# Kernel tuning notes

Hardware: AMD Instinct MI355X
Metric: run time of the kernel (lower is better)

## Reference

```python
import jax, jax.numpy as jnp
import numpy as np

B = 16; DEMO = 5; COND = 50; QOI = 50
L = DEMO * (COND + 2 * QOI)  # 750
D = 1024; H = 16; HD = D // H; NL = 6; DFF = 4096
IN_DIM = 5; OUT_DIM = 2; MAXPOS = max(COND, QOI)
NEG = -1e9


def _build_consts():
    # token types per demo segment: 0=cond, 1=qoi_kv, 2=qoi_k (query)
    types, demo, pos = [], [], []
    for d in range(DEMO):
        types += [0] * COND + [1] * QOI + [2] * QOI
        demo += [d] * (COND + 2 * QOI)
        pos += list(range(COND)) + list(range(QOI)) + list(range(QOI))
    t = np.array(types); g = np.array(demo); p = np.array(pos)
    ti, tj = t[:, None], t[None, :]
    gi, gj = g[:, None], g[None, :]
    eye = np.arange(L)[:, None] == np.arange(L)[None, :]
    prev = (gj < gi) & (tj < 2)                      # attend to cond/qoi_kv of earlier demos
    same = (gj == gi) & ((tj == 0) | ((ti == 1) & (tj == 1)) | ((ti == 2) & eye))
    mask = prev | same                               # True = allowed
    out_idx = np.where(t == 2)[0]                    # qoi_k positions -> outputs
    return mask, p, out_idx


def setup_inputs():
    key = jax.random.key(0)
    ks = jax.random.split(key, 10)
    mask, pos, out_idx = _build_consts()
    s = 0.02
    return {
        'sequence': jax.random.normal(ks[0], (B, L, IN_DIM), jnp.float32),
        'pre_W': jax.random.normal(ks[1], (IN_DIM, D), jnp.float32) * s,
        'pre_b': jnp.zeros((D,), jnp.float32),
        'pe_table': jax.random.normal(ks[2], (MAXPOS, D), jnp.float32) * s,
        'Wqkv': jax.random.normal(ks[3], (NL, D, 3 * D), jnp.float32) * s,
        'bqkv': jnp.zeros((NL, 3 * D), jnp.float32),
        'Wo': jax.random.normal(ks[4], (NL, D, D), jnp.float32) * s,
        'bo': jnp.zeros((NL, D), jnp.float32),
        'ln1_g': jnp.ones((NL, D), jnp.float32), 'ln1_b': jnp.zeros((NL, D), jnp.float32),
        'ln2_g': jnp.ones((NL, D), jnp.float32), 'ln2_b': jnp.zeros((NL, D), jnp.float32),
        'W1': jax.random.normal(ks[5], (NL, D, DFF), jnp.float32) * s,
        'b1': jnp.zeros((NL, DFF), jnp.float32),
        'W2': jax.random.normal(ks[6], (NL, DFF, D), jnp.float32) * s,
        'b2': jnp.zeros((NL, D), jnp.float32),
        'post_W': jax.random.normal(ks[7], (D, OUT_DIM), jnp.float32) * s,
        'post_b': jnp.zeros((OUT_DIM,), jnp.float32),
        'basic_mask': jnp.asarray(mask),
        'index_pos': jnp.asarray(pos, jnp.int32),
        'out_idx': jnp.asarray(out_idx, jnp.int32),
    }


def _ln(x, g, b):
    m = jnp.mean(x, axis=-1, keepdims=True)
    v = jnp.var(x, axis=-1, keepdims=True)
    return (x - m) * jax.lax.rsqrt(v + 1e-5) * g + b


def _encoder(x, bias, Wqkv, bqkv, Wo, bo, ln1_g, ln1_b, ln2_g, ln2_b, W1, b1, W2, b2):
    scale = 1.0 / np.sqrt(HD)
    for l in range(NL):
        qkv = x @ Wqkv[l] + bqkv[l]                          # [B,L,3D]
        q, k, v = jnp.split(qkv, 3, axis=-1)
        hd = lambda t: t.reshape(B, L, H, HD).transpose(0, 2, 1, 3)
        q, k, v = hd(q), hd(k), hd(v)
        sc = jnp.einsum('bhqd,bhkd->bhqk', q, k) * scale + bias
        a = jax.nn.softmax(sc, axis=-1)
        o = jnp.einsum('bhqk,bhkd->bhqd', a, v).transpose(0, 2, 1, 3).reshape(B, L, D)
        x = _ln(x + o @ Wo[l] + bo[l], ln1_g[l], ln1_b[l])   # post-LN (torch default)
        h = jax.nn.gelu(x @ W1[l] + b1[l], approximate=False)
        x = _ln(x + h @ W2[l] + b2[l], ln2_g[l], ln2_b[l])
    return x


def reference(sequence, pre_W, pre_b, pe_table, Wqkv, bqkv, Wo, bo,
              ln1_g, ln1_b, ln2_g, ln2_b, W1, b1, W2, b2,
              post_W, post_b, basic_mask, index_pos, out_idx):
    x = sequence @ pre_W + pre_b + pe_table[index_pos]       # pre-projection + learned PE
    bias = jnp.where(basic_mask, 0.0, NEG)[None, None, :, :]  # ~basic_mask -> -inf additive
    x = _encoder(x, bias, Wqkv, bqkv, Wo, bo, ln1_g, ln1_b, ln2_g, ln2_b, W1, b1, W2, b2)
    y = x @ post_W + post_b                                  # [B,L,OUT_DIM]
    y = y[:, out_idx, :]                                     # select qoi_k outputs
    return y.reshape(B, DEMO, QOI, OUT_DIM)
```

## Files before the change

### kernel.cpp

```cpp
#include <hip/hip_runtime.h>


#define Bz  16
#define Lz  750
#define Dz  1024
#define Hz  16
#define HDz 64
#define NLz 6
#define DFFz 4096
#define Mz  (Bz*Lz)
#define VSTRIDE 768
#define QKVPART ((size_t)Bz*Hz*Lz*HDz)

typedef unsigned short u16;
typedef unsigned int   u32;
typedef unsigned long long u64;
typedef __attribute__((ext_vector_type(8))) short bf8;
typedef __attribute__((ext_vector_type(4))) float f4;
typedef __attribute__((ext_vector_type(4))) unsigned short u16x4;

__device__ __forceinline__ u16 f2b(float f){
  u32 u = __builtin_bit_cast(u32, f);
  u += 0x7fffu + ((u >> 16) & 1u);
  return (u16)(u >> 16);
}
__device__ __forceinline__ u32 cvtpk(float a, float b){
  u32 r;
  asm("v_cvt_pk_bf16_f32 %0, %1, %2" : "=v"(r) : "v"(a), "v"(b));
  return r;
}
__device__ __forceinline__ void glds16(const void* g, void* l){
  __builtin_amdgcn_global_load_lds((const __attribute__((address_space(1))) void*)g,
                                   (__attribute__((address_space(3))) void*)l, 16, 0, 0);
}

__global__ __launch_bounds__(256) void k_embed(const float* __restrict__ seq,
    const float* __restrict__ preW, const float* __restrict__ preb,
    const float* __restrict__ pe, float* __restrict__ x, u16* __restrict__ xb){
  const int m = blockIdx.x, t = threadIdx.x;
  const int l = m % Lz;
  const int r = l % 150;
  const int p = r < 50 ? r : (r < 100 ? r - 50 : r - 100);
  const float s0 = seq[m*5+0], s1 = seq[m*5+1], s2 = seq[m*5+2],
              s3 = seq[m*5+3], s4 = seq[m*5+4];
  const int d = t*4;
  f4 acc = *(const f4*)&preb[d];
  acc += *(const f4*)&pe[p*Dz + d];
  acc += s0 * *(const f4*)&preW[0*Dz + d];
  acc += s1 * *(const f4*)&preW[1*Dz + d];
  acc += s2 * *(const f4*)&preW[2*Dz + d];
  acc += s3 * *(const f4*)&preW[3*Dz + d];
  acc += s4 * *(const f4*)&preW[4*Dz + d];
  *(f4*)&x[(size_t)m*Dz + d] = acc;
  u16x4 hv = { f2b(acc.x), f2b(acc.y), f2b(acc.z), f2b(acc.w) };
  *(u16x4*)&xb[(size_t)m*Dz + d] = hv;
}

__global__ __launch_bounds__(256) void k_transpose(const float* __restrict__ W,
    u16* __restrict__ Wt, int K, int ldw){
  __shared__ float tile[32][33];
  const int tx = threadIdx.x, ty = threadIdx.y;
  const int n0 = blockIdx.x*32, k0 = blockIdx.y*32;
  #pragma unroll
  for (int i = 0; i < 4; i++){
    const int k = ty + i*8;
    tile[k][tx] = W[(size_t)(k0+k)*ldw + n0+tx];
  }
  __syncthreads();
  #pragma unroll
  for (int i = 0; i < 4; i++){
    const int n = ty + i*8;
    Wt[(size_t)(n0+n)*K + k0+tx] = f2b(tile[tx][n]);
  }
}

template<int EPI>
__global__ __launch_bounds__(256, 2) void k_gemm(
    const u16* __restrict__ A, const u16* __restrict__ Bt,
    int M, int N, int K, int lda, int ldc, int col0,
    const float* __restrict__ bias,
    float* __restrict__ xres, u16* __restrict__ outb, u16* __restrict__ vtb){
  __shared__ u16 As[128*64];
  __shared__ u16 Bs[128*64];
  const int t = threadIdx.x;
  const int m0 = blockIdx.x*128, n0 = blockIdx.y*128;
  const int w = t >> 6, lane = t & 63;
  const int wm = (w >> 1)*64, wn = (w & 1)*64;
  const int cl = lane & 15, g4 = lane >> 4;
  f4 acc[4][4] = {};
  const int srow = t >> 3, scol = (t & 7)*8;
  const int lds_off = srow*64 + scol;
  for (int k0 = 0; k0 < K; k0 += 64){
    #pragma unroll
    for (int c = 0; c < 4; c++){
      int ra = m0 + c*32 + srow; ra = ra < M ? ra : M-1;
      glds16(A + (size_t)ra*lda + k0 + scol, &As[c*2048 + lds_off]);
      const int rb = n0 + c*32 + srow;
      glds16(Bt + (size_t)rb*K + k0 + scol, &Bs[c*2048 + lds_off]);
    }
    __syncthreads();
    #pragma unroll
    for (int kk = 0; kk < 2; kk++){
      const int ko = kk*32 + g4*8;
      bf8 af[4], bfr[4];
      #pragma unroll
      for (int i = 0; i < 4; i++) af[i]  = *(const bf8*)&As[(wm + i*16 + cl)*64 + ko];
      #pragma unroll
      for (int j = 0; j < 4; j++) bfr[j] = *(const bf8*)&Bs[(wn + j*16 + cl)*64 + ko];
      #pragma unroll
      for (int i = 0; i < 4; i++)
        #pragma unroll
        for (int j = 0; j < 4; j++)
          acc[i][j] = __builtin_amdgcn_mfma_f32_16x16x32_bf16(af[i], bfr[j], acc[i][j], 0, 0, 0);
    }
    __syncthreads();
  }
  const int rl = g4*4;
  #pragma unroll
  for (int i = 0; i < 4; i++){
    #pragma unroll
    for (int j = 0; j < 4; j++){
      const int gn = n0 + wn + j*16 + cl;
      const float bsv = bias ? bias[gn] : 0.f;
      if constexpr (EPI == 0){
        const int part = gn >> 10;
        const int hh = (gn >> 6) & 15;
        const int dd = gn & 63;
        const int gm0 = m0 + wm + i*16 + rl;
        if (part == 2){
          if (gm0 + 3 < M){
            const int b = gm0 / Lz, lr0 = gm0 - b*Lz;
            const float v0 = acc[i][j][0] + bsv, v1 = acc[i][j][1] + bsv;
            const float v2 = acc[i][j][2] + bsv, v3 = acc[i][j][3] + bsv;
            if (lr0 <= Lz - 4){
              u32* dst = (u32*)&vtb[((size_t)(b*Hz + hh)*HDz + dd)*VSTRIDE + lr0];
              dst[0] = cvtpk(v0, v1);
              dst[1] = cvtpk(v2, v3);
            } else {
              #pragma unroll
              for (int r = 0; r < 4; r++){
                const int gm = gm0 + r;
                const int br = gm / Lz, lr = gm - br*Lz;
                vtb[((size_t)(br*Hz + hh)*HDz + dd)*VSTRIDE + lr] = f2b(acc[i][j][r] + bsv);
              }
            }
          }
        } else {
          #pragma unroll
          for (int r = 0; r < 4; r++){
            const int gm = gm0 + r;
            if (gm < M){
              const int b = gm / Lz, lr = gm - b*Lz;
              outb[(size_t)part*QKVPART + ((size_t)(b*Hz + hh)*Lz + lr)*HDz + dd]
                  = f2b(acc[i][j][r] + bsv);
            }
          }
        }
      } else {
        #pragma unroll
        for (int r = 0; r < 4; r++){
          const int gm = m0 + wm + i*16 + rl + r;
          if (gm < M){
            const float v = acc[i][j][r] + bsv;
            if constexpr (EPI == 1){
              xres[(size_t)gm*ldc + col0 + gn] += v;
            } else {
              const float ge = 0.5f*v*(1.0f + erff(v*0.70710678f));
              outb[(size_t)gm*ldc + col0 + gn] = f2b(ge);
            }
          }
        }
      }
    }
  }
}

__global__ __launch_bounds__(256) void k_attn(const u16* __restrict__ qb,
    const u16* __restrict__ kb, const u16* __restrict__ vt, u16* __restrict__ ob){
  __shared__ u32 Ps[4][1024];
  const int t = threadIdx.x, w = t >> 6, lane = t & 63;
  const int cl = lane & 15, g4 = lane >> 4;
  const int bh = blockIdx.y, b = bh >> 4, h = bh & 15;
  const int bx = blockIdx.x;
  const u16* qhp = qb + (size_t)bh*(Lz*HDz);
  const u16* khp = kb + (size_t)bh*(Lz*HDz);
  const u16* vhp = vt + (size_t)bh*(HDz*VSTRIDE);
  u32* myPs = &Ps[w][0];
  const float SC = 0.18033688011112042f;
  const f4 z4 = {0.f, 0.f, 0.f, 0.f};

  for (int half = 0; half < 2; half++){
    const int qt = half ? (5 - bx) : bx;
    const int q0 = qt*128 + w*32;
    bf8 qfr[2][2];
    int qi[2], gq[2], thr[2]; bool isv[2];
    #pragma unroll
    for (int qf = 0; qf < 2; qf++){
      const int q = q0 + qf*16 + cl;
      const int qc = q < Lz ? q : Lz-1;
      #pragma unroll
      for (int kk = 0; kk < 2; kk++)
        qfr[qf][kk] = *(const bf8*)&qhp[(size_t)qc*HDz + kk*32 + g4*8];
      qi[qf] = q;
      gq[qf] = q/150;
      const int rq = q - gq[qf]*150;
      const int tq = rq < 50 ? 0 : (rq < 100 ? 1 : 2);
      thr[qf] = (tq == 1) ? 100 : 50;
      isv[qf] = (tq == 2);
    }
    int qmax = q0 + 31; if (qmax > Lz-1) qmax = Lz-1;
    const int gqm = qmax/150;
    int kmax = gqm*150 + 100; if (qmax + 1 > kmax) kmax = qmax + 1;
    const int nt = (kmax + 63) >> 6;

    f4 oacc[4][2] = {};
    float mrun[2] = {-1e30f, -1e30f}, lrun[2] = {0.f, 0.f};

    for (int kt = 0; kt < nt; kt++){
      const int kstart = kt*64;
      f4 sacc[4][2];
      #pragma unroll
      for (int kk = 0; kk < 2; kk++){
        bf8 kfr[4];
        #pragma unroll
        for (int kf = 0; kf < 4; kf++)
          kfr[kf] = *(const bf8*)&khp[(size_t)(kstart + kf*16 + cl)*HDz + kk*32 + g4*8];
        #pragma unroll
        for (int kf = 0; kf < 4; kf++)
          #pragma unroll
          for (int qf = 0; qf < 2; qf++)
            sacc[kf][qf] = __builtin_amdgcn_mfma_f32_16x16x32_bf16(kfr[kf], qfr[qf][kk],
                             kk == 0 ? z4 : sacc[kf][qf], 0, 0, 0);
      }
      float own0 = -1e30f, own1 = -1e30f;
      #pragma unroll
      for (int kf = 0; kf < 4; kf++){
        #pragma unroll
        for (int rr = 0; rr < 4; rr++){
          const int k = kstart + kf*16 + g4*4 + rr;
          const int gk = k/150, rk = k - gk*150;
          #pragma unroll
          for (int qf = 0; qf < 2; qf++){
            const int lim = (gk < gq[qf]) ? 100 : ((gk == gq[qf]) ? thr[qf] : 0);
            const bool ok = (rk < lim) || (isv[qf] && k == qi[qf]);
            const float s = ok ? sacc[kf][qf][rr]*SC : -1e30f;
            sacc[kf][qf][rr] = s;
            if (qf == 0) own0 = fmaxf(own0, s); else own1 = fmaxf(own1, s);
          }
        }
      }
      own0 = fmaxf(own0, __shfl_xor(own0, 16)); own0 = fmaxf(own0, __shfl_xor(own0, 32));
      own1 = fmaxf(own1, __shfl_xor(own1, 16)); own1 = fmaxf(own1, __shfl_xor(own1, 32));
      const float mn0 = fmaxf(mrun[0], own0), mn1 = fmaxf(mrun[1], own1);
      const float sc0 = exp2f(mrun[0] - mn0), sc1 = exp2f(mrun[1] - mn1);
      float sum0 = 0.f, sum1 = 0.f;
      #pragma unroll
      for (int kf = 0; kf < 4; kf++){
        #pragma unroll
        for (int qf = 0; qf < 2; qf++){
          const float mn = qf ? mn1 : mn0;
          f4 p;
          #pragma unroll
          for (int rr = 0; rr < 4; rr++){
            p[rr] = exp2f(sacc[kf][qf][rr] - mn);
            if (qf == 0) sum0 += p[rr]; else sum1 += p[rr];
          }
          const u32 lo = cvtpk(p[0], p[1]);
          const u32 hi = cvtpk(p[2], p[3]);
          const int kk = kf >> 1;
          const int tg4 = ((kf & 1) << 1) | (g4 >> 1);
          const int widx = (qf*2 + kk)*256 + tg4*64 + cl*4 + (g4 & 1)*2;
          *(u64*)&myPs[widx] = ((u64)hi << 32) | lo;
        }
      }
      sum0 += __shfl_xor(sum0, 16); sum0 += __shfl_xor(sum0, 32);
      sum1 += __shfl_xor(sum1, 16); sum1 += __shfl_xor(sum1, 32);
      lrun[0] = lrun[0]*sc0 + sum0; mrun[0] = mn0;
      lrun[1] = lrun[1]*sc1 + sum1; mrun[1] = mn1;
      #pragma unroll
      for (int df = 0; df < 4; df++){
        oacc[df][0] *= sc0;
        oacc[df][1] *= sc1;
      }
      #pragma unroll
      for (int kk = 0; kk < 2; kk++){
        bf8 vfr[4];
        #pragma unroll
        for (int df = 0; df < 4; df++)
          vfr[df] = *(const bf8*)&vhp[(size_t)(df*16 + cl)*VSTRIDE + kstart + kk*32 + g4*8];
        bf8 pw[2];
        #pragma unroll
        for (int qf = 0; qf < 2; qf++)
          pw[qf] = *(const bf8*)&myPs[(qf*2 + kk)*256 + g4*64 + cl*4];
        #pragma unroll
        for (int df = 0; df < 4; df++)
          #pragma unroll
          for (int qf = 0; qf < 2; qf++)
            oacc[df][qf] = __builtin_amdgcn_mfma_f32_16x16x32_bf16(vfr[df], pw[qf], oacc[df][qf], 0, 0, 0);
      }
    }
    #pragma unroll
    for (int qf = 0; qf < 2; qf++){
      const int q = q0 + qf*16 + cl;
      if (q < Lz){
        const float inv = 1.f / lrun[qf];
        #pragma unroll
        for (int df = 0; df < 4; df++){
          u16x4 hv = { f2b(oacc[df][qf][0]*inv), f2b(oacc[df][qf][1]*inv),
                       f2b(oacc[df][qf][2]*inv), f2b(oacc[df][qf][3]*inv) };
          *(u16x4*)&ob[((size_t)b*Lz + q)*Dz + h*HDz + df*16 + g4*4] = hv;
        }
      }
    }
  }
}

__global__ __launch_bounds__(256) void k_ln(float* __restrict__ x, u16* __restrict__ xb,
    const float* __restrict__ g, const float* __restrict__ bb){
  const int m = blockIdx.x, t = threadIdx.x;
  float* xr = x + (size_t)m*Dz;
  f4 v = *(const f4*)&xr[t*4];
  float s = v.x + v.y + v.z + v.w;
  float q = v.x*v.x + v.y*v.y + v.z*v.z + v.w*v.w;
  #pragma unroll
  for (int off = 1; off < 64; off <<= 1){
    s += __shfl_xor(s, off);
    q += __shfl_xor(q, off);
  }
  __shared__ float ss[4], sq[4];
  const int w = t >> 6;
  if ((t & 63) == 0){ ss[w] = s; sq[w] = q; }
  __syncthreads();
  s = ss[0] + ss[1] + ss[2] + ss[3];
  q = sq[0] + sq[1] + sq[2] + sq[3];
  const float mean = s * (1.f/1024.f);
  const float var  = q * (1.f/1024.f) - mean*mean;
  const float rs = rsqrtf(var + 1e-5f);
  const f4 gg = *(const f4*)&g[t*4];
  const f4 bv = *(const f4*)&bb[t*4];
  f4 o;
  o.x = (v.x - mean)*rs*gg.x + bv.x;
  o.y = (v.y - mean)*rs*gg.y + bv.y;
  o.z = (v.z - mean)*rs*gg.z + bv.z;
  o.w = (v.w - mean)*rs*gg.w + bv.w;
  *(f4*)&xr[t*4] = o;
  u16x4 hv = { f2b(o.x), f2b(o.y), f2b(o.z), f2b(o.w) };
  *(u16x4*)&xb[(size_t)m*Dz + t*4] = hv;
}

__global__ __launch_bounds__(64) void k_out(const float* __restrict__ x,
    const float* __restrict__ pw, const float* __restrict__ pb, float* __restrict__ out){
  const int bid = blockIdx.x, lane = threadIdx.x;
  const int b = bid / 250, oi = bid - b*250;
  const int dd = oi / 50, qq = oi - dd*50;
  const int l = dd*150 + 100 + qq;
  const float* xr = x + ((size_t)b*Lz + l)*Dz;
  float a0 = 0.f, a1 = 0.f;
  #pragma unroll
  for (int c = 0; c < 4; c++){
    const int d = c*256 + lane*4;
    const f4 v  = *(const f4*)&xr[d];
    const f4 p0 = *(const f4*)&pw[2*d];
    const f4 p1 = *(const f4*)&pw[2*d + 4];
    a0 += v.x*p0.x + v.y*p0.z + v.z*p1.x + v.w*p1.z;
    a1 += v.x*p0.y + v.y*p0.w + v.z*p1.y + v.w*p1.w;
  }
  #pragma unroll
  for (int off = 32; off > 0; off >>= 1){
    a0 += __shfl_xor(a0, off);
    a1 += __shfl_xor(a1, off);
  }
  if (lane == 0){
    out[(size_t)bid*2 + 0] = a0 + pb[0];
    out[(size_t)bid*2 + 1] = a1 + pb[1];
  }
}

extern "C" void kernel_launch(void* const* d_in, const int* in_sizes, int n_in,
                              void* d_out, int out_size, void* d_ws, size_t ws_size,
                              hipStream_t stream){
  (void)in_sizes; (void)n_in; (void)out_size; (void)ws_size;
  const float* seq   = (const float*)d_in[0];
  const float* preW  = (const float*)d_in[1];
  const float* preb  = (const float*)d_in[2];
  const float* pe    = (const float*)d_in[3];
  const float* Wqkv  = (const float*)d_in[4];
  const float* bqkv  = (const float*)d_in[5];
  const float* Wo    = (const float*)d_in[6];
  const float* bo    = (const float*)d_in[7];
  const float* ln1g  = (const float*)d_in[8];
  const float* ln1b  = (const float*)d_in[9];
  const float* ln2g  = (const float*)d_in[10];
  const float* ln2b  = (const float*)d_in[11];
  const float* W1    = (const float*)d_in[12];
  const float* b1    = (const float*)d_in[13];
  const float* W2    = (const float*)d_in[14];
  const float* b2    = (const float*)d_in[15];
  const float* postW = (const float*)d_in[16];
  const float* postb = (const float*)d_in[17];
  float* out = (float*)d_out;

  char* ws = (char*)d_ws;
  float* x  = (float*)(ws + 0);
  u16*   xb = (u16*)(ws + 49152000);
  u16*   R  = (u16*)(ws + 73728000);
  u16* qB = R;
  u16* kB = R + QKVPART;
  u16* oB = R + 2*QKVPART;
  u16* vT = (u16*)(ws + 147456000);
  u16* wt = (u16*)(ws + 172621824);
  u16* hB = R;

  k_embed<<<Mz, 256, 0, stream>>>(seq, preW, preb, pe, x, xb);
  const dim3 tb(32, 8);
  for (int l = 0; l < NLz; l++){
    k_transpose<<<dim3(96, 32), tb, 0, stream>>>(Wqkv + (size_t)l*1024*3072, wt, 1024, 3072);
    k_gemm<0><<<dim3(94, 24), 256, 0, stream>>>(xb, wt, Mz, 3072, 1024, 1024, 0, 0,
                                                bqkv + l*3072, nullptr, qB, vT);
    k_attn<<<dim3(3, 256), 256, 0, stream>>>(qB, kB, vT, oB);
    k_transpose<<<dim3(32, 32), tb, 0, stream>>>(Wo + (size_t)l*1024*1024, wt, 1024, 1024);
    k_gemm<1><<<dim3(94, 8), 256, 0, stream>>>(oB, wt, Mz, 1024, 1024, 1024, 1024, 0,
                                               bo + l*1024, x, nullptr, nullptr);
    k_ln<<<Mz, 256, 0, stream>>>(x, xb, ln1g + l*1024, ln1b + l*1024);
    for (int off = 0; off < 4096; off += 2048){
      k_transpose<<<dim3(64, 32), tb, 0, stream>>>(W1 + (size_t)l*1024*4096 + off, wt, 1024, 4096);
      k_gemm<2><<<dim3(94, 16), 256, 0, stream>>>(xb, wt, Mz, 2048, 1024, 1024, 4096, off,
                                                  b1 + l*4096 + off, nullptr, hB, nullptr);
    }
    for (int koff = 0; koff < 4096; koff += 2048){
      k_transpose<<<dim3(32, 64), tb, 0, stream>>>(W2 + (size_t)l*4096*1024 + (size_t)koff*1024,
                                                   wt, 2048, 1024);
      k_gemm<1><<<dim3(94, 8), 256, 0, stream>>>(hB + koff, wt, Mz, 1024, 2048, 4096, 1024, 0,
                                                 koff == 0 ? (b2 + l*1024) : nullptr, x, nullptr, nullptr);
    }
    k_ln<<<Mz, 256, 0, stream>>>(x, xb, ln2g + l*1024, ln2b + l*1024);
  }
  k_out<<<4000, 64, 0, stream>>>(x, postW, postb, out);
}
```

Baseline: 4.329 ms.

## Use 256x256 GEMM tiles with double-buffered LDS, swizzle, and XCD-aware block remap

The GEMM tile grows from 128x128 with 256 threads to 256x256 with 512 threads, and each wave now computes 128x64. LDS is double-buffered so the next K-slice loads while the current one is computed, leaving one barrier per iteration. An XOR swizzle is applied to the LDS layout to reduce bank conflicts. The 1D grid is remapped so consecutive tiles land on the same XCD for L2 reuse. The goal is higher arithmetic intensity and hidden load latency, at the cost of 128KB LDS per block, heavier register pressure and fewer blocks for tail balancing.

Measured after the change: 5.340 ms. 1.23x slower.

```diff
diff --git a/kernel.cpp b/kernel.cpp
--- a/kernel.cpp
+++ b/kernel.cpp
@@ -9,6 +9,7 @@
 #define NLz 6
 #define DFFz 4096
 #define Mz  (Bz*Lz)
+#define MT  47
 #define VSTRIDE 768
 #define QKVPART ((size_t)Bz*Hz*Lz*HDz)
 
@@ -75,63 +76,94 @@
 }
 
 template<int EPI>
-__global__ __launch_bounds__(256, 2) void k_gemm(
+__global__ __launch_bounds__(512, 2) void k_gemm(
     const u16* __restrict__ A, const u16* __restrict__ Bt,
     int M, int N, int K, int lda, int ldc, int col0,
     const float* __restrict__ bias,
     float* __restrict__ xres, u16* __restrict__ outb, u16* __restrict__ vtb){
-  __shared__ u16 As[128*64];
-  __shared__ u16 Bs[128*64];
+  __shared__ u16 As[2][256*64];
+  __shared__ u16 Bs[2][256*64];
   const int t = threadIdx.x;
-  const int m0 = blockIdx.x*128, n0 = blockIdx.y*128;
+  int id = blockIdx.x;
+  {
+    const int nwg = gridDim.x;
+    const int q = nwg >> 3, r = nwg & 7;
+    const int xcd = id & 7, i = id >> 3;
+    id = (xcd < r ? xcd*(q+1) : r*(q+1) + (xcd - r)*q) + i;
+  }
+  const int m0 = (id % MT) * 256;
+  const int n0 = (id / MT) * 256;
   const int w = t >> 6, lane = t & 63;
-  const int wm = (w >> 1)*64, wn = (w & 1)*64;
+  const int wm = (w >> 2)*128, wn = (w & 3)*64;
   const int cl = lane & 15, g4 = lane >> 4;
-  f4 acc[4][4] = {};
-  const int srow = t >> 3, scol = (t & 7)*8;
-  const int lds_off = srow*64 + scol;
-  for (int k0 = 0; k0 < K; k0 += 64){
+
+  const int srow = t >> 3;
+  const int sg   = t & 7;
+  const int gsw  = (sg ^ (srow & 7)) * 8;
+  const int ldst = (srow*64 + sg*8);
+
+  f4 acc[8][4] = {};
+
+#define STAGE(c, kt) do {                                                         \
+    _Pragma("unroll")                                                             \
+    for (int ii = 0; ii < 4; ii++){                                               \
+      int ra = m0 + ii*64 + srow; if (ra >= M) ra = M-1;                          \
+      glds16(A  + (size_t)ra*lda + (kt)*64 + gsw, &As[c][ii*4096 + ldst]);        \
+      const int rb = n0 + ii*64 + srow;                                           \
+      glds16(Bt + (size_t)rb*K   + (kt)*64 + gsw, &Bs[c][ii*4096 + ldst]);        \
+    }                                                                             \
+  } while(0)
+
+#define COMPUTE(c) do {                                                           \
+    _Pragma("unroll")                                                             \
+    for (int kk = 0; kk < 2; kk++){                                               \
+      const int swz = ((kk*4 + g4) ^ (cl & 7)) * 8;                               \
+      bf8 bfr[4];                                                                 \
+      _Pragma("unroll")                                                           \
+      for (int nf = 0; nf < 4; nf++)                                              \
+        bfr[nf] = *(const bf8*)&Bs[c][(wn + nf*16 + cl)*64 + swz];                \
+      _Pragma("unroll")                                                           \
+      for (int mf = 0; mf < 8; mf++){                                             \
+        const bf8 af = *(const bf8*)&As[c][(wm + mf*16 + cl)*64 + swz];           \
+        _Pragma("unroll")                                                         \
+        for (int nf = 0; nf < 4; nf++)                                            \
+          acc[mf][nf] = __builtin_amdgcn_mfma_f32_16x16x32_bf16(af, bfr[nf],      \
+                                                               acc[mf][nf], 0, 0, 0); \
+      }                                                                           \
+    }                                                                             \
+  } while(0)
+
+  const int nt = K >> 6;
+  int cur = 0;
+  STAGE(0, 0);
+  __syncthreads();
+  for (int kt = 0; kt < nt - 1; kt++){
+    STAGE(cur ^ 1, kt + 1);
+    COMPUTE(cur);
+    __syncthreads();
+    cur ^= 1;
+  }
+  COMPUTE(cur);
+#undef STAGE
+#undef COMPUTE
+
+  const int rl = g4*4;
+  #pragma unroll
+  for (int mf = 0; mf < 8; mf++){
     #pragma unroll
-    for (int c = 0; c < 4; c++){
-      int ra = m0 + c*32 + srow; ra = ra < M ? ra : M-1;
-      glds16(A + (size_t)ra*lda + k0 + scol, &As[c*2048 + lds_off]);
-      const int rb = n0 + c*32 + srow;
-      glds16(Bt + (size_t)rb*K + k0 + scol, &Bs[c*2048 + lds_off]);
-    }
-    __syncthreads();
-    #pragma unroll
-    for (int kk = 0; kk < 2; kk++){
-      const int ko = kk*32 + g4*8;
-      bf8 af[4], bfr[4];
-      #pragma unroll
-      for (int i = 0; i < 4; i++) af[i]  = *(const bf8*)&As[(wm + i*16 + cl)*64 + ko];
-      #pragma unroll
-      for (int j = 0; j < 4; j++) bfr[j] = *(const bf8*)&Bs[(wn + j*16 + cl)*64 + ko];
-      #pragma unroll
-      for (int i = 0; i < 4; i++)
-        #pragma unroll
-        for (int j = 0; j < 4; j++)
-          acc[i][j] = __builtin_amdgcn_mfma_f32_16x16x32_bf16(af[i], bfr[j], acc[i][j], 0, 0, 0);
-    }
-    __syncthreads();
-  }
-  const int rl = g4*4;
-  #pragma unroll
-  for (int i = 0; i < 4; i++){
-    #pragma unroll
-    for (int j = 0; j < 4; j++){
-      const int gn = n0 + wn + j*16 + cl;
+    for (int nf = 0; nf < 4; nf++){
+      const int gn = n0 + wn + nf*16 + cl;
       const float bsv = bias ? bias[gn] : 0.f;
       if constexpr (EPI == 0){
         const int part = gn >> 10;
         const int hh = (gn >> 6) & 15;
         const int dd = gn & 63;
-        const int gm0 = m0 + wm + i*16 + rl;
+        const int gm0 = m0 + wm + mf*16 + rl;
         if (part == 2){
           if (gm0 + 3 < M){
             const int b = gm0 / Lz, lr0 = gm0 - b*Lz;
-            const float v0 = acc[i][j][0] + bsv, v1 = acc[i][j][1] + bsv;
-            const float v2 = acc[i][j][2] + bsv, v3 = acc[i][j][3] + bsv;
+            const float v0 = acc[mf][nf][0] + bsv, v1 = acc[mf][nf][1] + bsv;
+            const float v2 = acc[mf][nf][2] + bsv, v3 = acc[mf][nf][3] + bsv;
             if (lr0 <= Lz - 4){
               u32* dst = (u32*)&vtb[((size_t)(b*Hz + hh)*HDz + dd)*VSTRIDE + lr0];
               dst[0] = cvtpk(v0, v1);
@@ -141,7 +173,7 @@
               for (int r = 0; r < 4; r++){
                 const int gm = gm0 + r;
                 const int br = gm / Lz, lr = gm - br*Lz;
-                vtb[((size_t)(br*Hz + hh)*HDz + dd)*VSTRIDE + lr] = f2b(acc[i][j][r] + bsv);
+                vtb[((size_t)(br*Hz + hh)*HDz + dd)*VSTRIDE + lr] = f2b(acc[mf][nf][r] + bsv);
               }
             }
           }
@@ -152,16 +184,16 @@
             if (gm < M){
               const int b = gm / Lz, lr = gm - b*Lz;
               outb[(size_t)part*QKVPART + ((size_t)(b*Hz + hh)*Lz + lr)*HDz + dd]
-                  = f2b(acc[i][j][r] + bsv);
+                  = f2b(acc[mf][nf][r] + bsv);
             }
           }
         }
       } else {
         #pragma unroll
         for (int r = 0; r < 4; r++){
-          const int gm = m0 + wm + i*16 + rl + r;
+          const int gm = m0 + wm + mf*16 + rl + r;
           if (gm < M){
-            const float v = acc[i][j][r] + bsv;
+            const float v = acc[mf][nf][r] + bsv;
             if constexpr (EPI == 1){
               xres[(size_t)gm*ldc + col0 + gn] += v;
             } else {
@@ -415,23 +447,23 @@
   const dim3 tb(32, 8);
   for (int l = 0; l < NLz; l++){
     k_transpose<<<dim3(96, 32), tb, 0, stream>>>(Wqkv + (size_t)l*1024*3072, wt, 1024, 3072);
-    k_gemm<0><<<dim3(94, 24), 256, 0, stream>>>(xb, wt, Mz, 3072, 1024, 1024, 0, 0,
-                                                bqkv + l*3072, nullptr, qB, vT);
+    k_gemm<0><<<MT*12, 512, 0, stream>>>(xb, wt, Mz, 3072, 1024, 1024, 0, 0,
+                                         bqkv + l*3072, nullptr, qB, vT);
     k_attn<<<dim3(3, 256), 256, 0, stream>>>(qB, kB, vT, oB);
     k_transpose<<<dim3(32, 32), tb, 0, stream>>>(Wo + (size_t)l*1024*1024, wt, 1024, 1024);
-    k_gemm<1><<<dim3(94, 8), 256, 0, stream>>>(oB, wt, Mz, 1024, 1024, 1024, 1024, 0,
-                                               bo + l*1024, x, nullptr, nullptr);
+    k_gemm<1><<<MT*4, 512, 0, stream>>>(oB, wt, Mz, 1024, 1024, 1024, 1024, 0,
+                                        bo + l*1024, x, nullptr, nullptr);
     k_ln<<<Mz, 256, 0, stream>>>(x, xb, ln1g + l*1024, ln1b + l*1024);
     for (int off = 0; off < 4096; off += 2048){
       k_transpose<<<dim3(64, 32), tb, 0, stream>>>(W1 + (size_t)l*1024*4096 + off, wt, 1024, 4096);
-      k_gemm<2><<<dim3(94, 16), 256, 0, stream>>>(xb, wt, Mz, 2048, 1024, 1024, 4096, off,
-                                                  b1 + l*4096 + off, nullptr, hB, nullptr);
+      k_gemm<2><<<MT*8, 512, 0, stream>>>(xb, wt, Mz, 2048, 1024, 1024, 4096, off,
+                                          b1 + l*4096 + off, nullptr, hB, nullptr);
     }
     for (int koff = 0; koff < 4096; koff += 2048){
       k_transpose<<<dim3(32, 64), tb, 0, stream>>>(W2 + (size_t)l*4096*1024 + (size_t)koff*1024,
                                                    wt, 2048, 1024);
-      k_gemm<1><<<dim3(94, 8), 256, 0, stream>>>(hB + koff, wt, Mz, 1024, 2048, 4096, 1024, 0,
-                                                 koff == 0 ? (b2 + l*1024) : nullptr, x, nullptr, nullptr);
+      k_gemm<1><<<MT*4, 512, 0, stream>>>(hB + koff, wt, Mz, 1024, 2048, 4096, 1024, 0,
+                                          koff == 0 ? (b2 + l*1024) : nullptr, x, nullptr, nullptr);
     }
     k_ln<<<Mz, 256, 0, stream>>>(x, xb, ln2g + l*1024, ln2b + l*1024);
   }
```

## Precompute attention mask bitmap and split attention into single-wave blocks

Applied to the files above, without the earlier changes.

Adds a one-time kernel that builds a per-query, per-64-key-tile bitmask of allowed positions, so the attention inner loop uses bit tests instead of per-element integer division and comparisons. The attention kernel becomes 64-thread single-wave blocks over 32-query chunks (12x256 grid, still pairing chunks for balance), with launch bounds raised for occupancy. It also adds s_setprio around the MFMA phases to favour matrix issue. Masked entries now get zero probability after exp rather than -inf scores, which could misbehave only if a row had no allowed keys in a tile while its running max comes from masked scores.

Measured after the change: 4.302 ms. About the same (-0.6%).

```diff
diff --git a/kernel.cpp b/kernel.cpp
--- a/kernel.cpp
+++ b/kernel.cpp
@@ -32,6 +32,25 @@
 __device__ __forceinline__ void glds16(const void* g, void* l){
   __builtin_amdgcn_global_load_lds((const __attribute__((address_space(1))) void*)g,
                                    (__attribute__((address_space(3))) void*)l, 16, 0, 0);
+}
+
+__global__ __launch_bounds__(256) void k_mask(u64* __restrict__ mb){
+  const int idx = blockIdx.x*256 + threadIdx.x;
+  if (idx >= Lz*12) return;
+  const int q = idx / 12, kt = idx - q*12;
+  const int gq = q/150, rq = q - gq*150;
+  const int tq = rq < 50 ? 0 : (rq < 100 ? 1 : 2);
+  u64 m = 0;
+  for (int j = 0; j < 64; j++){
+    const int k = kt*64 + j;
+    if (k >= Lz) break;
+    const int gk = k/150, rk = k - gk*150;
+    const int tk = rk < 50 ? 0 : (rk < 100 ? 1 : 2);
+    const bool prev = (gk < gq) && (tk < 2);
+    const bool same = (gk == gq) && ((tk == 0) || (tq == 1 && tk == 1) || (tq == 2 && k == q));
+    if (prev || same) m |= (1ull << j);
+  }
+  mb[idx] = m;
 }
 
 __global__ __launch_bounds__(256) void k_embed(const float* __restrict__ seq,
@@ -175,38 +194,32 @@
   }
 }
 
-__global__ __launch_bounds__(256) void k_attn(const u16* __restrict__ qb,
-    const u16* __restrict__ kb, const u16* __restrict__ vt, u16* __restrict__ ob){
-  __shared__ u32 Ps[4][1024];
-  const int t = threadIdx.x, w = t >> 6, lane = t & 63;
-  const int cl = lane & 15, g4 = lane >> 4;
+__global__ __launch_bounds__(64, 3) void k_attn(const u16* __restrict__ qb,
+    const u16* __restrict__ kb, const u16* __restrict__ vt,
+    const u64* __restrict__ mb, u16* __restrict__ ob){
+  __shared__ u32 Ps[1024];
+  const int t = threadIdx.x;
+  const int cl = t & 15, g4 = t >> 4;
   const int bh = blockIdx.y, b = bh >> 4, h = bh & 15;
   const int bx = blockIdx.x;
   const u16* qhp = qb + (size_t)bh*(Lz*HDz);
   const u16* khp = kb + (size_t)bh*(Lz*HDz);
   const u16* vhp = vt + (size_t)bh*(HDz*VSTRIDE);
-  u32* myPs = &Ps[w][0];
   const float SC = 0.18033688011112042f;
   const f4 z4 = {0.f, 0.f, 0.f, 0.f};
 
   for (int half = 0; half < 2; half++){
-    const int qt = half ? (5 - bx) : bx;
-    const int q0 = qt*128 + w*32;
+    const int c = half ? (23 - bx) : bx;
+    const int q0 = c*32;
     bf8 qfr[2][2];
-    int qi[2], gq[2], thr[2]; bool isv[2];
+    int qc[2];
     #pragma unroll
     for (int qf = 0; qf < 2; qf++){
       const int q = q0 + qf*16 + cl;
-      const int qc = q < Lz ? q : Lz-1;
+      qc[qf] = q < Lz ? q : Lz-1;
       #pragma unroll
       for (int kk = 0; kk < 2; kk++)
-        qfr[qf][kk] = *(const bf8*)&qhp[(size_t)qc*HDz + kk*32 + g4*8];
-      qi[qf] = q;
-      gq[qf] = q/150;
-      const int rq = q - gq[qf]*150;
-      const int tq = rq < 50 ? 0 : (rq < 100 ? 1 : 2);
-      thr[qf] = (tq == 1) ? 100 : 50;
-      isv[qf] = (tq == 2);
+        qfr[qf][kk] = *(const bf8*)&qhp[(size_t)qc[qf]*HDz + kk*32 + g4*8];
     }
     int qmax = q0 + 31; if (qmax > Lz-1) qmax = Lz-1;
     const int gqm = qmax/150;
@@ -218,7 +231,14 @@
 
     for (int kt = 0; kt < nt; kt++){
       const int kstart = kt*64;
+      u32 mlo[2], mhi[2];
+      #pragma unroll
+      for (int qf = 0; qf < 2; qf++){
+        const u64 m = mb[qc[qf]*12 + kt];
+        mlo[qf] = (u32)m; mhi[qf] = (u32)(m >> 32);
+      }
       f4 sacc[4][2];
+      __builtin_amdgcn_s_setprio(1);
       #pragma unroll
       for (int kk = 0; kk < 2; kk++){
         bf8 kfr[4];
@@ -232,21 +252,16 @@
             sacc[kf][qf] = __builtin_amdgcn_mfma_f32_16x16x32_bf16(kfr[kf], qfr[qf][kk],
                              kk == 0 ? z4 : sacc[kf][qf], 0, 0, 0);
       }
+      __builtin_amdgcn_s_setprio(0);
       float own0 = -1e30f, own1 = -1e30f;
       #pragma unroll
       for (int kf = 0; kf < 4; kf++){
         #pragma unroll
         for (int rr = 0; rr < 4; rr++){
-          const int k = kstart + kf*16 + g4*4 + rr;
-          const int gk = k/150, rk = k - gk*150;
-          #pragma unroll
-          for (int qf = 0; qf < 2; qf++){
-            const int lim = (gk < gq[qf]) ? 100 : ((gk == gq[qf]) ? thr[qf] : 0);
-            const bool ok = (rk < lim) || (isv[qf] && k == qi[qf]);
-            const float s = ok ? sacc[kf][qf][rr]*SC : -1e30f;
-            sacc[kf][qf][rr] = s;
-            if (qf == 0) own0 = fmaxf(own0, s); else own1 = fmaxf(own1, s);
-          }
+          const float s0 = sacc[kf][0][rr]*SC;
+          const float s1 = sacc[kf][1][rr]*SC;
+          sacc[kf][0][rr] = s0; sacc[kf][1][rr] = s1;
+          own0 = fmaxf(own0, s0); own1 = fmaxf(own1, s1);
         }
       }
       own0 = fmaxf(own0, __shfl_xor(own0, 16)); own0 = fmaxf(own0, __shfl_xor(own0, 32));
@@ -259,10 +274,13 @@
         #pragma unroll
         for (int qf = 0; qf < 2; qf++){
           const float mn = qf ? mn1 : mn0;
+          const u32 w16 = ((kf & 2) ? mhi[qf] : mlo[qf]) >> ((kf & 1)*16);
+          const u32 wq = w16 >> (g4*4);
           f4 p;
           #pragma unroll
           for (int rr = 0; rr < 4; rr++){
-            p[rr] = exp2f(sacc[kf][qf][rr] - mn);
+            const float pe = exp2f(sacc[kf][qf][rr] - mn);
+            p[rr] = ((wq >> rr) & 1u) ? pe : 0.f;
             if (qf == 0) sum0 += p[rr]; else sum1 += p[rr];
           }
           const u32 lo = cvtpk(p[0], p[1]);
@@ -270,7 +288,7 @@
           const int kk = kf >> 1;
           const int tg4 = ((kf & 1) << 1) | (g4 >> 1);
           const int widx = (qf*2 + kk)*256 + tg4*64 + cl*4 + (g4 & 1)*2;
-          *(u64*)&myPs[widx] = ((u64)hi << 32) | lo;
+          *(u64*)&Ps[widx] = ((u64)hi << 32) | lo;
         }
       }
       sum0 += __shfl_xor(sum0, 16); sum0 += __shfl_xor(sum0, 32);
@@ -282,6 +300,7 @@
         oacc[df][0] *= sc0;
         oacc[df][1] *= sc1;
       }
+      __builtin_amdgcn_s_setprio(1);
       #pragma unroll
       for (int kk = 0; kk < 2; kk++){
         bf8 vfr[4];
@@ -291,13 +310,14 @@
         bf8 pw[2];
         #pragma unroll
         for (int qf = 0; qf < 2; qf++)
-          pw[qf] = *(const bf8*)&myPs[(qf*2 + kk)*256 + g4*64 + cl*4];
+          pw[qf] = *(const bf8*)&Ps[(qf*2 + kk)*256 + g4*64 + cl*4];
         #pragma unroll
         for (int df = 0; df < 4; df++)
           #pragma unroll
           for (int qf = 0; qf < 2; qf++)
             oacc[df][qf] = __builtin_amdgcn_mfma_f32_16x16x32_bf16(vfr[df], pw[qf], oacc[df][qf], 0, 0, 0);
       }
+      __builtin_amdgcn_s_setprio(0);
     }
     #pragma unroll
     for (int qf = 0; qf < 2; qf++){
@@ -409,15 +429,17 @@
   u16* oB = R + 2*QKVPART;
   u16* vT = (u16*)(ws + 147456000);
   u16* wt = (u16*)(ws + 172621824);
+  u64* mbp = (u64*)(ws + 178913280);
   u16* hB = R;
 
+  k_mask<<<36, 256, 0, stream>>>(mbp);
   k_embed<<<Mz, 256, 0, stream>>>(seq, preW, preb, pe, x, xb);
   const dim3 tb(32, 8);
   for (int l = 0; l < NLz; l++){
     k_transpose<<<dim3(96, 32), tb, 0, stream>>>(Wqkv + (size_t)l*1024*3072, wt, 1024, 3072);
     k_gemm<0><<<dim3(94, 24), 256, 0, stream>>>(xb, wt, Mz, 3072, 1024, 1024, 0, 0,
                                                 bqkv + l*3072, nullptr, qB, vT);
-    k_attn<<<dim3(3, 256), 256, 0, stream>>>(qB, kB, vT, oB);
+    k_attn<<<dim3(12, 256), 64, 0, stream>>>(qB, kB, vT, mbp, oB);
     k_transpose<<<dim3(32, 32), tb, 0, stream>>>(Wo + (size_t)l*1024*1024, wt, 1024, 1024);
     k_gemm<1><<<dim3(94, 8), 256, 0, stream>>>(oB, wt, Mz, 1024, 1024, 1024, 1024, 0,
                                                bo + l*1024, x, nullptr, nullptr);
```
